# Kernel tuning notes

Measured on AMD Instinct MI355X. Metric: run time of the kernel, lower is better.

The kernel has to match this reference:

```python
import jax, jax.numpy as jnp
import numpy as np
from jax import lax

K = 32768          # queue size
C = 100            # num_classes == len(cls_num_list1)
B = 1024           # batch size (features.shape[0] - K)
D = 128            # embedding dim
ALPHA = 0.05; BETA = 1.0; GAMMA = 1.0; SUPT = 1.0
T = 0.07; BASE_T = 0.07   # base_temperature defaults to temperature
SMOOTH = 0.0; EPS = 1e-12


def setup_inputs() -> dict:
    key = jax.random.key(0)
    k1, k2, k3, k4 = jax.random.split(key, 4)
    features = jax.random.normal(k1, (B + K, D), dtype=jnp.float32)
    features = features / jnp.linalg.norm(features, axis=1, keepdims=True)  # contrastive feats are L2-normalized
    centers = jax.random.normal(k2, (C, D), dtype=jnp.float32)
    centers = centers / jnp.linalg.norm(centers, axis=1, keepdims=True)
    sup_logits = jax.random.normal(k3, (B, C), dtype=jnp.float32)
    labels = jax.random.randint(k4, (B + K,), 0, C, dtype=jnp.int32)
    return {"features": features, "sup_logits": sup_logits, "centers": centers, "labels": labels}


def _loss(features, sup_logits, centers, labels):
    f32 = features.dtype
    lab_c = jnp.arange(C, dtype=labels.dtype)
    lab1 = jnp.concatenate([labels[:B], lab_c])                 # [B+C]
    mask = (labels[:B, None] == labels[None, :]).astype(f32)    # [B, B+K]
    mask1 = (lab1[:B, None] == lab1[None, :]).astype(f32)       # [B, B+C]
    # class counts over batch+queue (batch_cls_count) and batch+centers (batch_cls_count1)
    cls_count = jnp.zeros((C,), f32).at[labels].add(1.0)
    cls_count1 = jnp.zeros((C,), f32).at[lab1].add(1.0)
    diag = jnp.arange(B)
    logits_mask = jnp.ones((B, B + K), f32).at[diag, diag].set(0.0)
    logits_mask1 = jnp.ones((B, B + C), f32).at[diag, diag].set(0.0)
    mask = mask * logits_mask
    mask1 = mask1 * logits_mask1

    # ---- branch 1: batch anchors vs [batch, class centers] ----
    feats1 = jnp.concatenate([features[:B], centers], axis=0)   # [B+C, D]
    logits1 = (features[:B] @ feats1.T) / T                     # [B, B+C]
    logits1 = logits1 - lax.stop_gradient(logits1.max(axis=1, keepdims=True))
    exp1 = jnp.exp(logits1) * logits_mask1
    w1 = cls_count1[lab1][None, :] - mask1                      # per-instance class weight
    denom1 = (exp1 / w1).sum(axis=1, keepdims=True)
    log_prob1 = logits1 - jnp.log(denom1 + EPS)
    loss1 = -jnp.mean((mask1 * log_prob1).sum(1) / mask1.sum(1))

    # ---- branch 2: [sup_logits, batch anchors vs batch+queue] ----
    adc = (features[:B] @ features.T) / T                       # [B, B+K]
    logits = jnp.concatenate([sup_logits / SUPT, adc], axis=1)  # [B, C+B+K] (self.weight is None)
    logits = logits - lax.stop_gradient(logits.max(axis=1, keepdims=True))
    one_hot = jax.nn.one_hot(labels[:B], C, dtype=f32)
    one_hot = SMOOTH / (C - 1) * (1.0 - one_hot) + (1.0 - SMOOTH) * one_hot
    mask_full = jnp.concatenate([one_hot * BETA, mask * ALPHA], axis=1)
    lmask_full = jnp.concatenate([jnp.ones((B, C), f32), GAMMA * logits_mask], axis=1)
    expl = jnp.exp(logits) * lmask_full
    lab_full = jnp.concatenate([lab_c, labels])                 # [C+B+K]
    w = cls_count[lab_full][None, :] - mask_full
    denom = (expl / w).sum(axis=1, keepdims=True)
    log_prob = logits - jnp.log(denom + EPS)
    loss2 = -(T / BASE_T) * jnp.mean((mask_full * log_prob).sum(1) / mask_full.sum(1))
    return loss1 + loss2


def reference(features, sup_logits, centers, labels):
    return _loss(features, sup_logits, centers, labels)
```

## Files before the change

kernel.cpp:

```cpp
#include <hip/hip_runtime.h>
#include <math.h>

#define KQ   32768
#define CC   100
#define BB   1024
#define DD   128
#define NTOT (BB + KQ)
#define CB_CENT 1056
#define NCB  1060
#define NHIST 33
#define NCG2 132
#define CG_SUP 141
#define NSL  141
#define NCI  18

#define INV_T  14.285714285714286f
#define K2E    20.609929f
#define ALPHA  0.05f
#define EPSV   1e-12f

typedef __attribute__((ext_vector_type(8)))  short          short8;
typedef __attribute__((ext_vector_type(8)))  unsigned short ushort8;
typedef __attribute__((ext_vector_type(16))) float          float16;

__device__ __forceinline__ unsigned short f2bf_rne(float f) {
    unsigned int u = __float_as_uint(f);
    return (unsigned short)((u + 0x7FFFu + ((u >> 16) & 1u)) >> 16);
}


__global__ __launch_bounds__(256) void prep_k(const float* __restrict__ feats,
                                              const float* __restrict__ centers,
                                              const int* __restrict__ labels,
                                              unsigned short* __restrict__ X2,
                                              int* __restrict__ cntP,
                                              int* __restrict__ cntB) {
    const int b = blockIdx.x, t = threadIdx.x;
    if (b >= NCB) {
        const int h = b - NCB;
        __shared__ int hA[CC], hB[CC];
        if (t < CC) { hA[t] = 0; hB[t] = 0; }
        __syncthreads();
        const int base = h * 1024;
#pragma unroll
        for (int q = 0; q < 4; ++q) {
            int l = labels[base + q * 256 + t];
            atomicAdd(&hA[l], 1);
            if (h == 0) atomicAdd(&hB[l], 1);
        }
        __syncthreads();
        if (t < 128) {
            cntP[h * 128 + t] = (t < CC) ? hA[t] : 0;
            if (h == 0) cntB[t] = (t < CC) ? hB[t] : 0;
        }
        return;
    }
    __shared__ unsigned short sm[8 * 66 * 8];
    const int cb = b;
    const int rl = t >> 3, c8 = t & 7;
    const int r = cb * 32 + rl;
    const float* src;
    if (r < NTOT)            src = &feats[(size_t)r * DD];
    else if (r < NTOT + CC)  src = &centers[(size_t)(r - NTOT) * DD];
    else                     src = nullptr;
#pragma unroll
    for (int s = 0; s < 2; ++s) {
        const int c8p = c8 + 8 * s;
        float v[8];
        if (src) {
            const float4* p = (const float4*)(src + c8p * 8);
            float4 q0 = p[0], q1 = p[1];
            v[0]=q0.x; v[1]=q0.y; v[2]=q0.z; v[3]=q0.w;
            v[4]=q1.x; v[5]=q1.y; v[6]=q1.z; v[7]=q1.w;
        } else {
#pragma unroll
            for (int j = 0; j < 8; ++j) v[j] = 0.f;
        }
        ushort8 H;
#pragma unroll
        for (int m = 0; m < 8; ++m) H[m] = f2bf_rne(v[m]);
        const int ks = c8p >> 1, lh = c8p & 1;
        *(ushort8*)&sm[(ks * 66 + rl + 32 * lh) * 8] = H;
    }
    __syncthreads();
    ushort8* dst = (ushort8*)((char*)X2 + (size_t)cb * 8192);
#pragma unroll
    for (int j = 0; j < 2; ++j) {
        const int idx = j * 256 + t;
        const int ks = idx >> 6, ln2 = idx & 63;
        dst[idx] = *(const ushort8*)&sm[(ks * 66 + ln2) * 8];
    }
}

__global__ __launch_bounds__(128) void tables_k(
    const int* __restrict__ cntP, const int* __restrict__ cntB,
    float2* __restrict__ wA, float2* __restrict__ w1, float2* __restrict__ wS,
    float* __restrict__ cAf, int* __restrict__ cBi) {
    const int t = threadIdx.x;
    int s = 0;
#pragma unroll
    for (int h = 0; h < NHIST; ++h) s += cntP[h * 128 + t];
    float cf = (float)s;
    float rn = (s > 0) ? __builtin_amdgcn_rcpf(cf) : 0.f;
    float dr = (s > 0) ? (__builtin_amdgcn_rcpf(cf - ALPHA) - rn) : 0.f;
    wA[t] = make_float2(rn, dr);
    wS[t] = make_float2(__builtin_amdgcn_rcpf(cf),
                        __builtin_amdgcn_rcpf(fmaxf(cf - 1.f, 1.f)));
    int sb = cntB[t];
    float c1 = (float)(sb + 1);
    float r1 = __builtin_amdgcn_rcpf(c1);
    w1[t] = make_float2(r1, __builtin_amdgcn_rcpf(fmaxf(c1 - 1.f, 1.f)) - r1);
    cAf[t] = cf;
    cBi[t] = sb;
}

__device__ __forceinline__ void epi_tile(
    const float16& acc, int cb, int lc, float rn, float drm, bool checkDiag,
    int half, int ln, int growbase, const int* rlab, float* sS, float* sN)
{
    const int ccol = cb * 32 + ln;
#pragma unroll
    for (int reg = 0; reg < 16; ++reg) {
        int ro = (reg & 3) + 8 * (reg >> 2) + 4 * half;
        float a  = acc[reg];
        float mf = (lc == rlab[reg]) ? 1.f : 0.f;
        float wgt = fmaf(mf, drm, rn);
        if (checkDiag) {
            bool d = (ccol == growbase + ro);
            wgt = d ? 0.f : wgt;
            mf  = d ? 0.f : mf;
        }
        float e = exp2f(fmaf(a, K2E, -K2E));
        sS[reg] = fmaf(e, wgt, sS[reg]);
        sN[reg] = fmaf(mf, a, sN[reg]);
    }
}

__device__ __forceinline__ void pair_tiles(
    const char* Xb, int cb0, int cb1,
    int lc0, float rn0, float drm0, bool dg0,
    int lc1, float rn1, float drm1, bool dg1,
    int lane, int half, int ln, int growbase,
    const short8* Ah, const int* rlab, float* sS, float* sN)
{
    const size_t b0 = (size_t)cb0 * 8192 + (size_t)lane * 16;
    const size_t b1 = (size_t)cb1 * 8192 + (size_t)lane * 16;
    float16 a0, a1;
#pragma unroll
    for (int reg = 0; reg < 16; ++reg) { a0[reg] = 0.f; a1[reg] = 0.f; }
#pragma unroll
    for (int ks = 0; ks < 8; ++ks) {
        short8 B0 = *(const short8*)(Xb + b0 + (size_t)ks * 1024);
        short8 B1 = *(const short8*)(Xb + b1 + (size_t)ks * 1024);
        a0 = __builtin_amdgcn_mfma_f32_32x32x16_bf16(Ah[ks], B0, a0, 0, 0, 0);
        a1 = __builtin_amdgcn_mfma_f32_32x32x16_bf16(Ah[ks], B1, a1, 0, 0, 0);
    }
    epi_tile(a0, cb0, lc0, rn0, drm0, dg0, half, ln, growbase, rlab, sS, sN);
    epi_tile(a1, cb1, lc1, rn1, drm1, dg1, half, ln, growbase, rlab, sS, sN);
}

__global__ __launch_bounds__(64, 2) void gemm_k(
    const unsigned short* __restrict__ X2, const int* __restrict__ labels,
    const float2* __restrict__ wA, const float2* __restrict__ w1,
    const float2* __restrict__ wS, const float* __restrict__ sup,
    float* __restrict__ pS, float* __restrict__ pN,
    float* __restrict__ supS, float* __restrict__ supLi) {
    const int b = blockIdx.x;
    const int xcd = b & 7, u = b >> 3;
    const int ci = u >> 5, rb = u & 31;
    const int cg = xcd + 8 * ci;
    if (cg > CG_SUP) return;

    const int lane = threadIdx.x & 63;
    const int half = lane >> 5, ln = lane & 31;
    const char* Xb = (const char*)X2;

    if (cg == CG_SUP) {
        const int c0 = lane, c1 = lane + 64;
        float2 t0 = wS[c0];
        float rA0 = t0.x, rAm0 = t0.y;
        float rA1 = 0.f, rAm1 = 0.f;
        if (lane < 36) { float2 t1 = wS[c1]; rA1 = t1.x; rAm1 = t1.y; }
        for (int rr = 0; rr < 32; ++rr) {
            int row = rb * 32 + rr;
            int li = labels[row];
            const float* srow = &sup[(size_t)row * CC];
            float v0 = srow[c0];
            float s = __expf(v0 - INV_T) * ((c0 == li) ? rAm0 : rA0);
            float liv = (c0 == li) ? v0 : 0.f;
            if (lane < 36) {
                float v1 = srow[c1];
                s += __expf(v1 - INV_T) * ((c1 == li) ? rAm1 : rA1);
                liv += (c1 == li) ? v1 : 0.f;
            }
#pragma unroll
            for (int off = 1; off < 64; off <<= 1) {
                s += __shfl_xor(s, off, 64);
                liv += __shfl_xor(liv, off, 64);
            }
            if (lane == 0) { supS[row] = s; supLi[row] = liv; }
        }
        return;
    }

    const int growbase = rb * 32;
    short8 Ah[8];
    {
        size_t abase = (size_t)rb * 8192 + (size_t)lane * 16;
#pragma unroll
        for (int ks = 0; ks < 8; ++ks)
            Ah[ks] = *(const short8*)(Xb + abase + (size_t)ks * 1024);
    }
    int rlab[16];
#pragma unroll
    for (int reg = 0; reg < 16; ++reg) {
        int ro = (reg & 3) + 8 * (reg >> 2) + 4 * half;
        rlab[reg] = labels[growbase + ro];
    }
    float sS[16], sN[16];
#pragma unroll
    for (int reg = 0; reg < 16; ++reg) { sS[reg] = 0.f; sN[reg] = 0.f; }

    const bool isB2 = (cg < NCG2);
    const int t1 = cg - NCG2;
    if (isB2) {
#pragma unroll
        for (int p = 0; p < 4; ++p) {
            const int cb0 = cg * 8 + 2 * p, cb1 = cb0 + 1;
            int lc0 = labels[cb0 * 32 + ln];
            int lc1 = labels[cb1 * 32 + ln];
            float2 wv0 = wA[lc0], wv1 = wA[lc1];
            pair_tiles(Xb, cb0, cb1, lc0, wv0.x, wv0.y, cb0 == rb,
                       lc1, wv1.x, wv1.y, cb1 == rb,
                       lane, half, ln, growbase, Ah, rlab, sS, sN);
        }
    } else {
        const bool isBatch = (t1 < 8);
#pragma unroll
        for (int p = 0; p < 2; ++p) {
            int cb0, cb1, lc0, lc1;
            if (isBatch) {
                cb0 = t1 * 4 + 2 * p; cb1 = cb0 + 1;
                lc0 = labels[cb0 * 32 + ln];
                lc1 = labels[cb1 * 32 + ln];
            } else {
                cb0 = CB_CENT + 2 * p; cb1 = cb0 + 1;
                int q0 = cb0 * 32 + ln - NTOT, q1 = cb1 * 32 + ln - NTOT;
                lc0 = (q0 < CC) ? q0 : -1;
                lc1 = (q1 < CC) ? q1 : -1;
            }
            float2 wv0 = w1[(lc0 >= 0) ? lc0 : 0];
            float2 wv1 = w1[(lc1 >= 0) ? lc1 : 0];
            float rn0  = (lc0 >= 0) ? wv0.x : 0.f;
            float drm0 = (lc0 >= 0) ? wv0.y : 0.f;
            float rn1v  = (lc1 >= 0) ? wv1.x : 0.f;
            float drm1v = (lc1 >= 0) ? wv1.y : 0.f;
            pair_tiles(Xb, cb0, cb1, lc0, rn0, drm0, isBatch && (cb0 == rb),
                       lc1, rn1v, drm1v, isBatch && (cb1 == rb),
                       lane, half, ln, growbase, Ah, rlab, sS, sN);
        }
    }
    const int slice = isB2 ? cg : (NCG2 + t1);
#pragma unroll
    for (int reg = 0; reg < 16; ++reg) {
        float a = sS[reg], c = sN[reg];
#pragma unroll
        for (int off = 1; off < 32; off <<= 1) {
            a += __shfl_xor(a, off, 64);
            c += __shfl_xor(c, off, 64);
        }
        if (ln == 0) {
            int ro = (reg & 3) + 8 * (reg >> 2) + 4 * half;
            int grow = growbase + ro;
            pS[(size_t)slice * BB + grow] = a;
            pN[(size_t)slice * BB + grow] = c;
        }
    }
}

__global__ __launch_bounds__(1024) void finalize_k(
    const int* __restrict__ labels,
    const float* __restrict__ cAf, const int* __restrict__ cBi,
    const float* __restrict__ pS, const float* __restrict__ pN,
    const float* __restrict__ supS, const float* __restrict__ supLi,
    float* __restrict__ out) {
    const int t = threadIdx.x;
    __shared__ float cA_s[128];
    __shared__ int   cB_s[128];
    if (t < 128) { cA_s[t] = cAf[t]; cB_s[t] = cBi[t]; }
    __syncthreads();
    const int li = labels[t];
    float S2 = supS[t], N2 = 0.f;
#pragma unroll 4
    for (int c = 0; c < NCG2; ++c) {
        S2 += pS[(size_t)c * BB + t];
        N2 += pN[(size_t)c * BB + t];
    }
    float S1 = 0.f, N1v = 0.f;
#pragma unroll
    for (int c = NCG2; c < NSL; ++c) {
        S1 += pS[(size_t)c * BB + t];
        N1v += pN[(size_t)c * BB + t];
    }
    N2 *= INV_T; N1v *= INV_T;
    float sli = supLi[t];
    float cA = cA_s[li];
    float msum2 = fmaf(ALPHA, cA - 1.f, 1.f);
    float loss2 = -(fmaf(ALPHA, N2, sli) / msum2 - INV_T - logf(S2 + EPSV));
    float loss1 = -(N1v / (float)cB_s[li] - INV_T - logf(S1 + EPSV));
    float s = loss1 + loss2;
    __shared__ float buf[16];
#pragma unroll
    for (int off = 1; off < 64; off <<= 1) s += __shfl_xor(s, off, 64);
    if ((t & 63) == 0) buf[t >> 6] = s;
    __syncthreads();
    if (t < 64) {
        float x = (t < 16) ? buf[t] : 0.f;
#pragma unroll
        for (int off = 1; off < 16; off <<= 1) x += __shfl_xor(x, off, 64);
        if (t == 0) out[0] = x / (float)BB;
    }
}

extern "C" void kernel_launch(void* const* d_in, const int* in_sizes, int n_in,
                              void* d_out, int out_size, void* d_ws, size_t ws_size,
                              hipStream_t stream) {
    const float* feats   = (const float*)d_in[0];
    const float* sup     = (const float*)d_in[1];
    const float* centers = (const float*)d_in[2];
    const int*   labels  = (const int*)d_in[3];
    float* out = (float*)d_out;
    char*  wsb = (char*)d_ws;

    const size_t X2_BYTES = (size_t)NCB * 8192;
    unsigned short* X2 = (unsigned short*)wsb;
    char* base2 = wsb + X2_BYTES;
    int* cntP = (int*)base2;
    int* cntB = cntP + NHIST * 128;
    float2* wA = (float2*)(cntB + 128);
    float2* w1 = wA + 128;
    float2* wS = w1 + 128;
    float*  cAf = (float*)(wS + 128);
    int*    cBi = (int*)(cAf + 128);
    float* pS = (float*)(cBi + 128);
    float* pN = pS + (size_t)NSL * BB;
    float* supS  = pN + (size_t)NSL * BB;
    float* supLi = supS + BB;

    prep_k<<<NCB + NHIST, 256, 0, stream>>>(feats, centers, labels, X2, cntP, cntB);
    tables_k<<<1, 128, 0, stream>>>(cntP, cntB, wA, w1, wS, cAf, cBi);
    gemm_k<<<8 * 32 * NCI, 64, 0, stream>>>(X2, labels, wA, w1, wS, sup,
                                            pS, pN, supS, supLi);
    finalize_k<<<1, 1024, 0, stream>>>(labels, cAf, cBi, pS, pN, supS, supLi, out);
}
```

Before: 134.4 us.

## Share column tiles across 4 waves via double-buffered LDS and split finalize reduction

The GEMM kernel now uses 256-thread blocks in which four waves, each owning a different 32-row block, share column tiles loaded cooperatively into a double-buffered LDS area. Each wave previously fetched B tiles straight from global memory on its own. The next tile is prefetched into registers while the current one is processed. The single-block finalize is split into a 32-block per-row reduction plus a tiny final kernel, which adds a launch in exchange for more parallelism. Per-iteration __syncthreads and losing the paired MFMA interleave may offset the reduced global traffic.

```diff
diff --git a/kernel.cpp b/kernel.cpp
--- a/kernel.cpp
+++ b/kernel.cpp
@@ -12,7 +12,6 @@
 #define NCG2 132
 #define CG_SUP 141
 #define NSL  141
-#define NCI  18
 
 #define INV_T  14.285714285714286f
 #define K2E    20.609929f
@@ -136,43 +135,21 @@
     }
 }
 
-__device__ __forceinline__ void pair_tiles(
-    const char* Xb, int cb0, int cb1,
-    int lc0, float rn0, float drm0, bool dg0,
-    int lc1, float rn1, float drm1, bool dg1,
-    int lane, int half, int ln, int growbase,
-    const short8* Ah, const int* rlab, float* sS, float* sN)
-{
-    const size_t b0 = (size_t)cb0 * 8192 + (size_t)lane * 16;
-    const size_t b1 = (size_t)cb1 * 8192 + (size_t)lane * 16;
-    float16 a0, a1;
-#pragma unroll
-    for (int reg = 0; reg < 16; ++reg) { a0[reg] = 0.f; a1[reg] = 0.f; }
-#pragma unroll
-    for (int ks = 0; ks < 8; ++ks) {
-        short8 B0 = *(const short8*)(Xb + b0 + (size_t)ks * 1024);
-        short8 B1 = *(const short8*)(Xb + b1 + (size_t)ks * 1024);
-        a0 = __builtin_amdgcn_mfma_f32_32x32x16_bf16(Ah[ks], B0, a0, 0, 0, 0);
-        a1 = __builtin_amdgcn_mfma_f32_32x32x16_bf16(Ah[ks], B1, a1, 0, 0, 0);
-    }
-    epi_tile(a0, cb0, lc0, rn0, drm0, dg0, half, ln, growbase, rlab, sS, sN);
-    epi_tile(a1, cb1, lc1, rn1, drm1, dg1, half, ln, growbase, rlab, sS, sN);
-}
-
-__global__ __launch_bounds__(64, 2) void gemm_k(
+__global__ __launch_bounds__(256, 2) void gemm_k(
     const unsigned short* __restrict__ X2, const int* __restrict__ labels,
     const float2* __restrict__ wA, const float2* __restrict__ w1,
     const float2* __restrict__ wS, const float* __restrict__ sup,
     float* __restrict__ pS, float* __restrict__ pN,
     float* __restrict__ supS, float* __restrict__ supLi) {
     const int b = blockIdx.x;
-    const int xcd = b & 7, u = b >> 3;
-    const int ci = u >> 5, rb = u & 31;
-    const int cg = xcd + 8 * ci;
+    const int xcd = b & 7, rgrp = (b >> 3) & 7, chunk = b >> 6;
+    const int cg = chunk * 8 + xcd;
     if (cg > CG_SUP) return;
 
-    const int lane = threadIdx.x & 63;
+    const int tid = threadIdx.x;
+    const int w = tid >> 6, lane = tid & 63;
     const int half = lane >> 5, ln = lane & 31;
+    const int rb = rgrp * 4 + w;
     const char* Xb = (const char*)X2;
 
     if (cg == CG_SUP) {
@@ -180,7 +157,7 @@
         float2 t0 = wS[c0];
         float rA0 = t0.x, rAm0 = t0.y;
         float rA1 = 0.f, rAm1 = 0.f;
-        if (lane < 36) { float2 t1 = wS[c1]; rA1 = t1.x; rAm1 = t1.y; }
+        if (lane < 36) { float2 t1v = wS[c1]; rA1 = t1v.x; rAm1 = t1v.y; }
         for (int rr = 0; rr < 32; ++rr) {
             int row = rb * 32 + rr;
             int li = labels[row];
@@ -203,6 +180,8 @@
         return;
     }
 
+    __shared__ char sm[2 * 8192];
+
     const int growbase = rb * 32;
     short8 Ah[8];
     {
@@ -223,103 +202,129 @@
 
     const bool isB2 = (cg < NCG2);
     const int t1 = cg - NCG2;
-    if (isB2) {
-#pragma unroll
-        for (int p = 0; p < 4; ++p) {
-            const int cb0 = cg * 8 + 2 * p, cb1 = cb0 + 1;
-            int lc0 = labels[cb0 * 32 + ln];
-            int lc1 = labels[cb1 * 32 + ln];
-            float2 wv0 = wA[lc0], wv1 = wA[lc1];
-            pair_tiles(Xb, cb0, cb1, lc0, wv0.x, wv0.y, cb0 == rb,
-                       lc1, wv1.x, wv1.y, cb1 == rb,
-                       lane, half, ln, growbase, Ah, rlab, sS, sN);
-        }
-    } else {
-        const bool isBatch = (t1 < 8);
-#pragma unroll
-        for (int p = 0; p < 2; ++p) {
-            int cb0, cb1, lc0, lc1;
-            if (isBatch) {
-                cb0 = t1 * 4 + 2 * p; cb1 = cb0 + 1;
-                lc0 = labels[cb0 * 32 + ln];
-                lc1 = labels[cb1 * 32 + ln];
-            } else {
-                cb0 = CB_CENT + 2 * p; cb1 = cb0 + 1;
-                int q0 = cb0 * 32 + ln - NTOT, q1 = cb1 * 32 + ln - NTOT;
-                lc0 = (q0 < CC) ? q0 : -1;
-                lc1 = (q1 < CC) ? q1 : -1;
-            }
-            float2 wv0 = w1[(lc0 >= 0) ? lc0 : 0];
-            float2 wv1 = w1[(lc1 >= 0) ? lc1 : 0];
-            float rn0  = (lc0 >= 0) ? wv0.x : 0.f;
-            float drm0 = (lc0 >= 0) ? wv0.y : 0.f;
-            float rn1v  = (lc1 >= 0) ? wv1.x : 0.f;
-            float drm1v = (lc1 >= 0) ? wv1.y : 0.f;
-            pair_tiles(Xb, cb0, cb1, lc0, rn0, drm0, isBatch && (cb0 == rb),
-                       lc1, rn1v, drm1v, isBatch && (cb1 == rb),
-                       lane, half, ln, growbase, Ah, rlab, sS, sN);
-        }
-    }
+    const bool isBatch = isB2 || (t1 < 8);
+    const int NIT = isB2 ? 8 : 4;
+    const int cb0 = isB2 ? cg * 8 : (t1 < 8 ? t1 * 4 : CB_CENT);
+
+    const int soff = (w * 2) * 1024 + lane * 16;
+
+    {
+        const char* src = Xb + (size_t)cb0 * 8192 + soff;
+        short8 s0 = *(const short8*)src;
+        short8 s1 = *(const short8*)(src + 1024);
+        *(short8*)&sm[soff] = s0;
+        *(short8*)&sm[soff + 1024] = s1;
+    }
+    __syncthreads();
+
+    for (int i = 0; i < NIT; ++i) {
+        const int cb = cb0 + i;
+        short8 st0, st1;
+        const bool more = (i + 1 < NIT);
+        if (more) {
+            const char* src = Xb + (size_t)(cb + 1) * 8192 + soff;
+            st0 = *(const short8*)src;
+            st1 = *(const short8*)(src + 1024);
+        }
+        int lc; float rn, drm; bool dg;
+        if (isBatch) {
+            lc = labels[cb * 32 + ln];
+            float2 wv = isB2 ? wA[lc] : w1[lc];
+            rn = wv.x; drm = wv.y; dg = (cb == rb);
+        } else {
+            int q = cb * 32 + ln - NTOT;
+            lc = (q < CC) ? q : -1;
+            float2 wv = w1[(lc >= 0) ? lc : 0];
+            rn  = (lc >= 0) ? wv.x : 0.f;
+            drm = (lc >= 0) ? wv.y : 0.f;
+            dg = false;
+        }
+        const char* Bp = &sm[(i & 1) * 8192 + lane * 16];
+        float16 a;
+#pragma unroll
+        for (int reg = 0; reg < 16; ++reg) a[reg] = 0.f;
+#pragma unroll
+        for (int ks = 0; ks < 8; ++ks) {
+            short8 Bf = *(const short8*)(Bp + ks * 1024);
+            a = __builtin_amdgcn_mfma_f32_32x32x16_bf16(Ah[ks], Bf, a, 0, 0, 0);
+        }
+        epi_tile(a, cb, lc, rn, drm, dg, half, ln, growbase, rlab, sS, sN);
+        if (more) {
+            char* d = &sm[((i + 1) & 1) * 8192 + soff];
+            *(short8*)d = st0;
+            *(short8*)(d + 1024) = st1;
+        }
+        __syncthreads();
+    }
+
     const int slice = isB2 ? cg : (NCG2 + t1);
 #pragma unroll
     for (int reg = 0; reg < 16; ++reg) {
-        float a = sS[reg], c = sN[reg];
+        float av = sS[reg], c = sN[reg];
 #pragma unroll
         for (int off = 1; off < 32; off <<= 1) {
-            a += __shfl_xor(a, off, 64);
-            c += __shfl_xor(c, off, 64);
+            av += __shfl_xor(av, off, 64);
+            c  += __shfl_xor(c, off, 64);
         }
         if (ln == 0) {
             int ro = (reg & 3) + 8 * (reg >> 2) + 4 * half;
             int grow = growbase + ro;
-            pS[(size_t)slice * BB + grow] = a;
+            pS[(size_t)slice * BB + grow] = av;
             pN[(size_t)slice * BB + grow] = c;
         }
     }
 }
 
-__global__ __launch_bounds__(1024) void finalize_k(
+__global__ __launch_bounds__(256) void reduce_k(
     const int* __restrict__ labels,
     const float* __restrict__ cAf, const int* __restrict__ cBi,
     const float* __restrict__ pS, const float* __restrict__ pN,
     const float* __restrict__ supS, const float* __restrict__ supLi,
-    float* __restrict__ out) {
-    const int t = threadIdx.x;
-    __shared__ float cA_s[128];
-    __shared__ int   cB_s[128];
-    if (t < 128) { cA_s[t] = cAf[t]; cB_s[t] = cBi[t]; }
-    __syncthreads();
-    const int li = labels[t];
-    float S2 = supS[t], N2 = 0.f;
-#pragma unroll 4
-    for (int c = 0; c < NCG2; ++c) {
-        S2 += pS[(size_t)c * BB + t];
-        N2 += pN[(size_t)c * BB + t];
-    }
-    float S1 = 0.f, N1v = 0.f;
-#pragma unroll
-    for (int c = NCG2; c < NSL; ++c) {
-        S1 += pS[(size_t)c * BB + t];
-        N1v += pN[(size_t)c * BB + t];
-    }
-    N2 *= INV_T; N1v *= INV_T;
-    float sli = supLi[t];
-    float cA = cA_s[li];
-    float msum2 = fmaf(ALPHA, cA - 1.f, 1.f);
-    float loss2 = -(fmaf(ALPHA, N2, sli) / msum2 - INV_T - logf(S2 + EPSV));
-    float loss1 = -(N1v / (float)cB_s[li] - INV_T - logf(S1 + EPSV));
-    float s = loss1 + loss2;
-    __shared__ float buf[16];
+    float* __restrict__ partial) {
+    const int g = blockIdx.x, t = threadIdx.x;
+    const int rl = t >> 3, j = t & 7;
+    const int row = g * 32 + rl;
+    float S2 = 0.f, N2 = 0.f, S1 = 0.f, N1v = 0.f;
+    for (int c = j; c < NCG2; c += 8) {
+        S2 += pS[(size_t)c * BB + row];
+        N2 += pN[(size_t)c * BB + row];
+    }
+    for (int c = NCG2 + j; c < NSL; c += 8) {
+        S1  += pS[(size_t)c * BB + row];
+        N1v += pN[(size_t)c * BB + row];
+    }
+#pragma unroll
+    for (int off = 1; off < 8; off <<= 1) {
+        S2 += __shfl_xor(S2, off, 64);  N2  += __shfl_xor(N2, off, 64);
+        S1 += __shfl_xor(S1, off, 64);  N1v += __shfl_xor(N1v, off, 64);
+    }
+    float s = 0.f;
+    if (j == 0) {
+        int li = labels[row];
+        S2 += supS[row];
+        N2 *= INV_T; N1v *= INV_T;
+        float sli = supLi[row];
+        float cA = cAf[li];
+        float msum2 = fmaf(ALPHA, cA - 1.f, 1.f);
+        float loss2 = -(fmaf(ALPHA, N2, sli) / msum2 - INV_T - logf(S2 + EPSV));
+        float loss1 = -(N1v / (float)cBi[li] - INV_T - logf(S1 + EPSV));
+        s = loss1 + loss2;
+    }
 #pragma unroll
     for (int off = 1; off < 64; off <<= 1) s += __shfl_xor(s, off, 64);
+    __shared__ float buf[4];
     if ((t & 63) == 0) buf[t >> 6] = s;
     __syncthreads();
-    if (t < 64) {
-        float x = (t < 16) ? buf[t] : 0.f;
-#pragma unroll
-        for (int off = 1; off < 16; off <<= 1) x += __shfl_xor(x, off, 64);
-        if (t == 0) out[0] = x / (float)BB;
-    }
+    if (t == 0) partial[g] = (buf[0] + buf[1]) + (buf[2] + buf[3]);
+}
+
+__global__ __launch_bounds__(64) void final_k(const float* __restrict__ partial,
+                                              float* __restrict__ out) {
+    const int t = threadIdx.x;
+    float s = (t < 32) ? partial[t] : 0.f;
+#pragma unroll
+    for (int off = 1; off < 64; off <<= 1) s += __shfl_xor(s, off, 64);
+    if (t == 0) out[0] = s / (float)BB;
 }
 
 extern "C" void kernel_launch(void* const* d_in, const int* in_sizes, int n_in,
@@ -346,10 +351,12 @@
     float* pN = pS + (size_t)NSL * BB;
     float* supS  = pN + (size_t)NSL * BB;
     float* supLi = supS + BB;
+    float* partial = supLi + BB;
 
     prep_k<<<NCB + NHIST, 256, 0, stream>>>(feats, centers, labels, X2, cntP, cntB);
     tables_k<<<1, 128, 0, stream>>>(cntP, cntB, wA, w1, wS, cAf, cBi);
-    gemm_k<<<8 * 32 * NCI, 64, 0, stream>>>(X2, labels, wA, w1, wS, sup,
-                                            pS, pN, supS, supLi);
-    finalize_k<<<1, 1024, 0, stream>>>(labels, cAf, cBi, pS, pN, supS, supLi, out);
-}
+    gemm_k<<<18 * 64, 256, 0, stream>>>(X2, labels, wA, w1, wS, sup,
+                                        pS, pN, supS, supLi);
+    reduce_k<<<32, 256, 0, stream>>>(labels, cAf, cBi, pS, pN, supS, supLi, partial);
+    final_k<<<1, 64, 0, stream>>>(partial, out);
+}
```

Result: faster. 125.9 us (-6.3%).
